# Optimization experiments

Measured on AMD Instinct MI355X. Metric: run time of the kernel, lower is better.

## Reference

```python
import jax, jax.numpy as jnp
import numpy as np

B, S, D, H = 4, 2048, 256, 8
HD = D // H  # 32
SCALE = 1.0 / jnp.sqrt(256.0)  # module divides by sqrt(256.0), NOT sqrt(head_dim)


def setup_inputs() -> dict:
    key = jax.random.key(0)
    ks = jax.random.split(key, 11)
    inp = {
        "q_in": jax.random.normal(ks[0], (B, S, D), jnp.float32),
        "k_in": jax.random.normal(ks[1], (B, S, D), jnp.float32),
        "v_in": jax.random.normal(ks[2], (B, S, D), jnp.float32),
        # causal mask, broadcastable over batch and heads; every row has >=1 one
        "mask": jnp.tril(jnp.ones((S, S), jnp.float32))[None, None, :, :],
        "Wq": jax.random.normal(ks[3], (D, D), jnp.float32) * 0.05,
        "bq": jnp.zeros((D,), jnp.float32),
        "Wk": jax.random.normal(ks[4], (D, D), jnp.float32) * 0.05,
        "bk": jnp.zeros((D,), jnp.float32),
        "Wv": jax.random.normal(ks[5], (D, D), jnp.float32) * 0.05,
        "bv": jnp.zeros((D,), jnp.float32),
        "Wo": jax.random.normal(ks[6], (D, D), jnp.float32) * 0.05,
        "bo": jnp.zeros((D,), jnp.float32),
    }
    return inp


def _mask_softmax(x, mask):
    # faithful to module: exp (no max-subtraction), remask, normalize
    e = jnp.exp(x) * mask
    return e / jnp.sum(e, axis=-1, keepdims=True)


def reference(q_in, k_in, v_in, mask, Wq, bq, Wk, bk, Wv, bv, Wo, bo):
    Q = (q_in @ Wq + bq).reshape(B, S, H, HD)
    K = (k_in @ Wk + bk).reshape(B, S, H, HD)
    V = (v_in @ Wv + bv).reshape(B, S, H, HD)
    scores = jnp.einsum("bqhd,bkhd->bhqk", Q, K) * SCALE  # [B,H,S,S]
    scores = scores * mask  # module multiplies mask into scores first
    p = _mask_softmax(scores, mask)
    attn = jnp.einsum("bhqk,bkhd->bqhd", p, V).reshape(B, S, D)
    return attn @ Wo + bo
```

## Files before the change

kernel.cpp:

```cpp
#include <hip/hip_runtime.h>
#include <hip/hip_bf16.h>

#define BATCH 4
#define S_LEN 2048
#define D_MOD 256
#define NH 8
#define HDIM 32
#define SCALE_ 0.0625f

typedef short bf16x8 __attribute__((ext_vector_type(8)));
typedef short short4v __attribute__((ext_vector_type(4)));
typedef float f32x4 __attribute__((ext_vector_type(4)));

__device__ __forceinline__ short f2bf(float f) {
    __hip_bfloat16 h = __float2bfloat16(f);
    return *reinterpret_cast<short*>(&h);
}

__global__ __launch_bounds__(256) void wtrans_kernel(
    const float* __restrict__ Wq, const float* __restrict__ Wk,
    const float* __restrict__ Wv, const float* __restrict__ Wo,
    short* __restrict__ WT)
{
    const int wsel = blockIdx.x;
    const int k0 = blockIdx.y * 8;
    const float* W = wsel == 0 ? Wq : (wsel == 1 ? Wk : (wsel == 2 ? Wv : Wo));
    short* T = WT + (size_t)wsel * 256 * 256;
    int n = threadIdx.x;
    bf16x8 o;
    #pragma unroll
    for (int kk = 0; kk < 8; ++kk)
        o[kk] = f2bf(W[(size_t)(k0 + kk) * 256 + n]);
    *(bf16x8*)&T[(size_t)n * 256 + k0] = o;
}

__global__ __launch_bounds__(256) void qkv_proj_kernel(
    const float* __restrict__ q_in, const float* __restrict__ k_in,
    const float* __restrict__ v_in, const short* __restrict__ WT,
    const float* __restrict__ bq, const float* __restrict__ bk,
    const float* __restrict__ bv,
    short* __restrict__ Qp, short* __restrict__ Kp, short* __restrict__ Vt)
{
    __shared__ short lsA[32][264];
    const int mt = blockIdx.x;
    const int seg = blockIdx.y;
    const float* A = seg == 0 ? q_in : (seg == 1 ? k_in : v_in);
    const short* WTs = WT + (size_t)seg * 65536;
    const float* bias = seg == 0 ? bq : (seg == 1 ? bk : bv);
    const int m0 = mt * 32;
    const int tid = threadIdx.x;

    {
        const float4* A4 = (const float4*)(A + (size_t)m0 * D_MOD);
        #pragma unroll
        for (int i = 0; i < 8; ++i) {
            int f4 = tid + i * 256;
            int row = f4 >> 6, c4 = f4 & 63;
            float4 v = A4[f4];
            short4v o;
            o.x = f2bf(v.x); o.y = f2bf(v.y); o.z = f2bf(v.z); o.w = f2bf(v.w);
            *(short4v*)&lsA[row][c4 * 4] = o;
        }
    }
    __syncthreads();

    const int w = tid >> 6, l = tid & 63, g = l >> 4, r15 = l & 15;
    bf16x8 af[2][8];
    #pragma unroll
    for (int f = 0; f < 2; ++f)
        #pragma unroll
        for (int kk = 0; kk < 8; ++kk)
            af[f][kk] = *(const bf16x8*)&lsA[f * 16 + r15][kk * 32 + 8 * g];

    const int bidx = m0 >> 11;
    const int s_base = m0 & (S_LEN - 1);

    #pragma unroll
    for (int ntl = 0; ntl < 4; ++ntl) {
        int col = w * 64 + ntl * 16 + r15;
        f32x4 acc0 = {}, acc1 = {};
        #pragma unroll
        for (int kk = 0; kk < 8; ++kk) {
            bf16x8 b = *(const bf16x8*)&WTs[(size_t)col * 256 + kk * 32 + 8 * g];
            acc0 = __builtin_amdgcn_mfma_f32_16x16x32_bf16(af[0][kk], b, acc0, 0, 0, 0);
            acc1 = __builtin_amdgcn_mfma_f32_16x16x32_bf16(af[1][kk], b, acc1, 0, 0, 0);
        }
        float bval = bias[col];
        int h = col >> 5, hd = col & 31;
        if (seg < 2) {
            short* Out = seg == 0 ? Qp : Kp;
            short* Outh = Out + ((size_t)(bidx * NH + h) * S_LEN) * HDIM;
            #pragma unroll
            for (int r = 0; r < 4; ++r) {
                int s0 = s_base + 4 * g + r;
                Outh[(size_t)s0 * HDIM + hd]        = f2bf(acc0[r] + bval);
                Outh[(size_t)(s0 + 16) * HDIM + hd] = f2bf(acc1[r] + bval);
            }
        } else {
            short* Vh = Vt + ((size_t)(bidx * NH + h) * HDIM + hd) * S_LEN;
            short4v o0, o1;
            #pragma unroll
            for (int r = 0; r < 4; ++r) { o0[r] = f2bf(acc0[r] + bval); o1[r] = f2bf(acc1[r] + bval); }
            size_t s = s_base + 4 * g;
            *(short4v*)&Vh[s]      = o0;
            *(short4v*)&Vh[s + 16] = o1;
        }
    }
}

__global__ __launch_bounds__(256) void attn_kernel(
    const short* __restrict__ Qp, const short* __restrict__ Kp,
    const short* __restrict__ Vt, short* __restrict__ Ab)
{
    __shared__ char smem[18432];
    __shared__ float psl[4][2][16];
    short (*pl)[32][72] = (short(*)[32][72])smem;
    float (*comb)[32][33] = (float(*)[32][33])smem;

    const int idx = blockIdx.x;
    const int bh = 4 * (idx & 7) + ((idx >> 3) & 3);
    const int jq = 63 - (idx >> 5);
    const int b = bh >> 3, h = bh & 7;
    const int tid = threadIdx.x;
    const int w = tid >> 6, l = tid & 63, g = l >> 4, r15 = l & 15;
    const int q0 = jq * 32;

    const short* Qph = Qp + (size_t)bh * S_LEN * HDIM;
    const short* Kph = Kp + (size_t)bh * S_LEN * HDIM;
    const short* Vtp = Vt + (size_t)bh * HDIM * S_LEN;

    bf16x8 aq0 = *(const bf16x8*)&Qph[(size_t)(q0 + r15) * HDIM + 8 * g];
    bf16x8 aq1 = *(const bf16x8*)&Qph[(size_t)(q0 + 16 + r15) * HDIM + 8 * g];

    f32x4 oacc[2][2] = {};
    float ps0[4] = {}, ps1[4] = {};
    const f32x4 zero = {};
    const int ntiles = (q0 + 95) >> 6;

    bf16x8 bkb[4];
    {
        const int k0 = w * 64;
        if (w < ntiles) {
            #pragma unroll
            for (int n = 0; n < 4; ++n)
                bkb[n] = *(const bf16x8*)&Kph[(size_t)(k0 + n * 16 + r15) * HDIM + 8 * g];
        }
    }

    for (int kt = w; kt < ntiles; kt += 4) {
        const int k0 = kt * 64;
        const bool full = (k0 + 63) <= q0;
        bf16x8 bkn[4];
        const int ktn = kt + 4;
        if (ktn < ntiles) {
            const int k0n = ktn * 64;
            #pragma unroll
            for (int n = 0; n < 4; ++n)
                bkn[n] = *(const bf16x8*)&Kph[(size_t)(k0n + n * 16 + r15) * HDIM + 8 * g];
        }

        __builtin_amdgcn_s_setprio(1);
        f32x4 s0v[4], s1v[4];
        #pragma unroll
        for (int n = 0; n < 4; ++n) {
            s0v[n] = __builtin_amdgcn_mfma_f32_16x16x32_bf16(aq0, bkb[n], zero, 0, 0, 0);
            s1v[n] = __builtin_amdgcn_mfma_f32_16x16x32_bf16(aq1, bkb[n], zero, 0, 0, 0);
        }
        __builtin_amdgcn_s_setprio(0);

        #pragma unroll
        for (int n = 0; n < 4; ++n) {
            int key = k0 + n * 16 + r15;
            if (full) {
                #pragma unroll
                for (int r = 0; r < 4; ++r) {
                    float e0 = __expf(s0v[n][r] * SCALE_);
                    float e1 = __expf(s1v[n][r] * SCALE_);
                    ps0[r] += e0; ps1[r] += e1;
                    pl[w][4 * g + r][n * 16 + r15]      = f2bf(e0);
                    pl[w][16 + 4 * g + r][n * 16 + r15] = f2bf(e1);
                }
            } else {
                #pragma unroll
                for (int r = 0; r < 4; ++r) {
                    int qr = q0 + 4 * g + r;
                    float e0 = (key <= qr)      ? __expf(s0v[n][r] * SCALE_) : 0.0f;
                    float e1 = (key <= qr + 16) ? __expf(s1v[n][r] * SCALE_) : 0.0f;
                    ps0[r] += e0; ps1[r] += e1;
                    pl[w][4 * g + r][n * 16 + r15]      = f2bf(e0);
                    pl[w][16 + 4 * g + r][n * 16 + r15] = f2bf(e1);
                }
            }
        }

        __builtin_amdgcn_s_setprio(1);
        #pragma unroll
        for (int ks = 0; ks < 2; ++ks) {
            bf16x8 pa0 = *(const bf16x8*)&pl[w][r15][ks * 32 + 8 * g];
            bf16x8 pa1 = *(const bf16x8*)&pl[w][16 + r15][ks * 32 + 8 * g];
            #pragma unroll
            for (int n2 = 0; n2 < 2; ++n2) {
                bf16x8 bv = *(const bf16x8*)&Vtp[(size_t)(n2 * 16 + r15) * S_LEN + k0 + ks * 32 + 8 * g];
                oacc[0][n2] = __builtin_amdgcn_mfma_f32_16x16x32_bf16(pa0, bv, oacc[0][n2], 0, 0, 0);
                oacc[1][n2] = __builtin_amdgcn_mfma_f32_16x16x32_bf16(pa1, bv, oacc[1][n2], 0, 0, 0);
            }
        }
        __builtin_amdgcn_s_setprio(0);

        if (ktn < ntiles) {
            #pragma unroll
            for (int n = 0; n < 4; ++n) bkb[n] = bkn[n];
        }
    }

    #pragma unroll
    for (int r = 0; r < 4; ++r) {
        float v0 = ps0[r], v1 = ps1[r];
        v0 += __shfl_xor(v0, 1); v1 += __shfl_xor(v1, 1);
        v0 += __shfl_xor(v0, 2); v1 += __shfl_xor(v1, 2);
        v0 += __shfl_xor(v0, 4); v1 += __shfl_xor(v1, 4);
        v0 += __shfl_xor(v0, 8); v1 += __shfl_xor(v1, 8);
        ps0[r] = v0; ps1[r] = v1;
    }

    __syncthreads();
    #pragma unroll
    for (int n2 = 0; n2 < 2; ++n2) {
        #pragma unroll
        for (int r = 0; r < 4; ++r) {
            comb[w][4 * g + r][n2 * 16 + r15]      = oacc[0][n2][r];
            comb[w][16 + 4 * g + r][n2 * 16 + r15] = oacc[1][n2][r];
        }
    }
    if (r15 == 0) {
        #pragma unroll
        for (int r = 0; r < 4; ++r) {
            psl[w][0][4 * g + r] = ps0[r];
            psl[w][1][4 * g + r] = ps1[r];
        }
    }
    __syncthreads();

    {
        int q = tid >> 3, hd0 = (tid & 7) * 4;
        int qf = q >> 4, q15 = q & 15;
        float ps = psl[0][qf][q15] + psl[1][qf][q15] + psl[2][qf][q15] + psl[3][qf][q15];
        float inv = __fdividef(1.0f, ps);
        short4v o;
        #pragma unroll
        for (int j = 0; j < 4; ++j) {
            float v = comb[0][q][hd0 + j] + comb[1][q][hd0 + j]
                    + comb[2][q][hd0 + j] + comb[3][q][hd0 + j];
            o[j] = f2bf(v * inv);
        }
        *(short4v*)&Ab[((size_t)b * S_LEN + q0 + q) * D_MOD + h * HDIM + hd0] = o;
    }
}

__global__ __launch_bounds__(256) void out_proj_kernel(
    const short* __restrict__ Ab, const short* __restrict__ WTo,
    const float* __restrict__ bo, float* __restrict__ out)
{
    const int m0 = blockIdx.x * 32;
    const int tid = threadIdx.x;
    const int w = tid >> 6, l = tid & 63, g = l >> 4, r15 = l & 15;

    bf16x8 af[2][8];
    #pragma unroll
    for (int f = 0; f < 2; ++f)
        #pragma unroll
        for (int kk = 0; kk < 8; ++kk)
            af[f][kk] = *(const bf16x8*)&Ab[(size_t)(m0 + f * 16 + r15) * D_MOD + kk * 32 + 8 * g];

    #pragma unroll
    for (int ntl = 0; ntl < 4; ++ntl) {
        int col = w * 64 + ntl * 16 + r15;
        f32x4 acc0 = {}, acc1 = {};
        #pragma unroll
        for (int kk = 0; kk < 8; ++kk) {
            bf16x8 bfr = *(const bf16x8*)&WTo[(size_t)col * 256 + kk * 32 + 8 * g];
            acc0 = __builtin_amdgcn_mfma_f32_16x16x32_bf16(af[0][kk], bfr, acc0, 0, 0, 0);
            acc1 = __builtin_amdgcn_mfma_f32_16x16x32_bf16(af[1][kk], bfr, acc1, 0, 0, 0);
        }
        float bval = bo[col];
        #pragma unroll
        for (int r = 0; r < 4; ++r) {
            out[(size_t)(m0 + 4 * g + r) * D_MOD + col]      = acc0[r] + bval;
            out[(size_t)(m0 + 16 + 4 * g + r) * D_MOD + col] = acc1[r] + bval;
        }
    }
}

extern "C" void kernel_launch(void* const* d_in, const int* in_sizes, int n_in,
                              void* d_out, int out_size, void* d_ws, size_t ws_size,
                              hipStream_t stream) {
    const float* q_in = (const float*)d_in[0];
    const float* k_in = (const float*)d_in[1];
    const float* v_in = (const float*)d_in[2];
    const float* Wq = (const float*)d_in[4];
    const float* bq = (const float*)d_in[5];
    const float* Wk = (const float*)d_in[6];
    const float* bk = (const float*)d_in[7];
    const float* Wv = (const float*)d_in[8];
    const float* bv = (const float*)d_in[9];
    const float* Wo = (const float*)d_in[10];
    const float* bo = (const float*)d_in[11];
    float* out = (float*)d_out;

    const size_t NTOK = (size_t)BATCH * S_LEN * D_MOD;
    short* WT = (short*)d_ws;
    short* Qp = WT + 4 * 65536;
    short* Kp = Qp + NTOK;
    short* Vt = Kp + NTOK;
    short* Ab = Vt + NTOK;

    wtrans_kernel<<<dim3(4, 32), 256, 0, stream>>>(Wq, Wk, Wv, Wo, WT);
    qkv_proj_kernel<<<dim3(256, 3), 256, 0, stream>>>(
        q_in, k_in, v_in, WT, bq, bk, bv, Qp, Kp, Vt);
    attn_kernel<<<2048, 256, 0, stream>>>(Qp, Kp, Vt, Ab);
    out_proj_kernel<<<256, 256, 0, stream>>>(Ab, WT + 3 * 65536, bo, out);
}
```

Baseline: 71.61 us.

## Pair long and short causal query tiles per block, fold scale into Q

Each attention block now handles two 32-row query tiles, one near the end and one near the start of the sequence, so causal work is balanced across blocks and each K/V tile load serves both tiles. The grid is halved to 1024 blocks. The softmax scale times log2(e) is folded into Q during projection so the inner loop can use exp2f without a multiply. The K double-buffer prefetch is removed and V loads are hoisted ahead of the PV MFMAs. This adds more LDS use and more registers per block, which could reduce occupancy, and Q is rounded to bf16 after scaling, which slightly changes precision.

```diff
diff --git a/kernel.cpp b/kernel.cpp
--- a/kernel.cpp
+++ b/kernel.cpp
@@ -7,6 +7,7 @@
 #define NH 8
 #define HDIM 32
 #define SCALE_ 0.0625f
+#define QLOG2E 0.09016844f
 
 typedef short bf16x8 __attribute__((ext_vector_type(8)));
 typedef short short4v __attribute__((ext_vector_type(4)));
@@ -87,9 +88,16 @@
         }
         float bval = bias[col];
         int h = col >> 5, hd = col & 31;
-        if (seg < 2) {
-            short* Out = seg == 0 ? Qp : Kp;
-            short* Outh = Out + ((size_t)(bidx * NH + h) * S_LEN) * HDIM;
+        if (seg == 0) {
+            short* Outh = Qp + ((size_t)(bidx * NH + h) * S_LEN) * HDIM;
+            #pragma unroll
+            for (int r = 0; r < 4; ++r) {
+                int s0 = s_base + 4 * g + r;
+                Outh[(size_t)s0 * HDIM + hd]        = f2bf((acc0[r] + bval) * QLOG2E);
+                Outh[(size_t)(s0 + 16) * HDIM + hd] = f2bf((acc1[r] + bval) * QLOG2E);
+            }
+        } else if (seg == 1) {
+            short* Outh = Kp + ((size_t)(bidx * NH + h) * S_LEN) * HDIM;
             #pragma unroll
             for (int r = 0; r < 4; ++r) {
                 int s0 = s_base + 4 * g + r;
@@ -108,152 +116,183 @@
     }
 }
 
-__global__ __launch_bounds__(256) void attn_kernel(
+__global__ __launch_bounds__(256, 4) void attn_kernel(
     const short* __restrict__ Qp, const short* __restrict__ Kp,
     const short* __restrict__ Vt, short* __restrict__ Ab)
 {
-    __shared__ char smem[18432];
-    __shared__ float psl[4][2][16];
-    short (*pl)[32][72] = (short(*)[32][72])smem;
-    float (*comb)[32][33] = (float(*)[32][33])smem;
+    __shared__ short pl[4][64][72];
+    __shared__ float psl[4][4][16];
+    float (*comb)[64][33] = (float(*)[64][33])pl;
 
     const int idx = blockIdx.x;
     const int bh = 4 * (idx & 7) + ((idx >> 3) & 3);
-    const int jq = 63 - (idx >> 5);
+    const int t  = idx >> 5;
     const int b = bh >> 3, h = bh & 7;
     const int tid = threadIdx.x;
     const int w = tid >> 6, l = tid & 63, g = l >> 4, r15 = l & 15;
-    const int q0 = jq * 32;
+    const int q0b = (63 - t) * 32;
+    const int q0s = t * 32;
 
     const short* Qph = Qp + (size_t)bh * S_LEN * HDIM;
     const short* Kph = Kp + (size_t)bh * S_LEN * HDIM;
     const short* Vtp = Vt + (size_t)bh * HDIM * S_LEN;
 
-    bf16x8 aq0 = *(const bf16x8*)&Qph[(size_t)(q0 + r15) * HDIM + 8 * g];
-    bf16x8 aq1 = *(const bf16x8*)&Qph[(size_t)(q0 + 16 + r15) * HDIM + 8 * g];
-
-    f32x4 oacc[2][2] = {};
-    float ps0[4] = {}, ps1[4] = {};
+    bf16x8 aqb0 = *(const bf16x8*)&Qph[(size_t)(q0b + r15) * HDIM + 8 * g];
+    bf16x8 aqb1 = *(const bf16x8*)&Qph[(size_t)(q0b + 16 + r15) * HDIM + 8 * g];
+    bf16x8 aqs0 = *(const bf16x8*)&Qph[(size_t)(q0s + r15) * HDIM + 8 * g];
+    bf16x8 aqs1 = *(const bf16x8*)&Qph[(size_t)(q0s + 16 + r15) * HDIM + 8 * g];
+
+    f32x4 ob[2][2] = {}, os[2][2] = {};
+    float psb0[4] = {}, psb1[4] = {}, pss0[4] = {}, pss1[4] = {};
     const f32x4 zero = {};
-    const int ntiles = (q0 + 95) >> 6;
-
-    bf16x8 bkb[4];
-    {
-        const int k0 = w * 64;
-        if (w < ntiles) {
-            #pragma unroll
-            for (int n = 0; n < 4; ++n)
-                bkb[n] = *(const bf16x8*)&Kph[(size_t)(k0 + n * 16 + r15) * HDIM + 8 * g];
-        }
-    }
-
-    for (int kt = w; kt < ntiles; kt += 4) {
+    const int ntb = (q0b + 95) >> 6;
+    const int nts = (q0s + 95) >> 6;
+
+    for (int kt = w; kt < ntb; kt += 4) {
         const int k0 = kt * 64;
-        const bool full = (k0 + 63) <= q0;
-        bf16x8 bkn[4];
-        const int ktn = kt + 4;
-        if (ktn < ntiles) {
-            const int k0n = ktn * 64;
-            #pragma unroll
-            for (int n = 0; n < 4; ++n)
-                bkn[n] = *(const bf16x8*)&Kph[(size_t)(k0n + n * 16 + r15) * HDIM + 8 * g];
-        }
-
-        __builtin_amdgcn_s_setprio(1);
-        f32x4 s0v[4], s1v[4];
+        const bool son = kt < nts;
+        const bool fb = (k0 + 63) <= q0b;
+        const bool fs = (k0 + 63) <= q0s;
+
+        bf16x8 bk[4];
+        #pragma unroll
+        for (int n = 0; n < 4; ++n)
+            bk[n] = *(const bf16x8*)&Kph[(size_t)(k0 + n * 16 + r15) * HDIM + 8 * g];
+
         #pragma unroll
         for (int n = 0; n < 4; ++n) {
-            s0v[n] = __builtin_amdgcn_mfma_f32_16x16x32_bf16(aq0, bkb[n], zero, 0, 0, 0);
-            s1v[n] = __builtin_amdgcn_mfma_f32_16x16x32_bf16(aq1, bkb[n], zero, 0, 0, 0);
-        }
-        __builtin_amdgcn_s_setprio(0);
-
-        #pragma unroll
-        for (int n = 0; n < 4; ++n) {
-            int key = k0 + n * 16 + r15;
-            if (full) {
+            const int key = k0 + n * 16 + r15;
+            __builtin_amdgcn_s_setprio(1);
+            f32x4 s0 = __builtin_amdgcn_mfma_f32_16x16x32_bf16(aqb0, bk[n], zero, 0, 0, 0);
+            f32x4 s1 = __builtin_amdgcn_mfma_f32_16x16x32_bf16(aqb1, bk[n], zero, 0, 0, 0);
+            __builtin_amdgcn_s_setprio(0);
+            if (fb) {
                 #pragma unroll
                 for (int r = 0; r < 4; ++r) {
-                    float e0 = __expf(s0v[n][r] * SCALE_);
-                    float e1 = __expf(s1v[n][r] * SCALE_);
-                    ps0[r] += e0; ps1[r] += e1;
+                    float e0 = exp2f(s0[r]);
+                    float e1 = exp2f(s1[r]);
+                    psb0[r] += e0; psb1[r] += e1;
                     pl[w][4 * g + r][n * 16 + r15]      = f2bf(e0);
                     pl[w][16 + 4 * g + r][n * 16 + r15] = f2bf(e1);
                 }
             } else {
                 #pragma unroll
                 for (int r = 0; r < 4; ++r) {
-                    int qr = q0 + 4 * g + r;
-                    float e0 = (key <= qr)      ? __expf(s0v[n][r] * SCALE_) : 0.0f;
-                    float e1 = (key <= qr + 16) ? __expf(s1v[n][r] * SCALE_) : 0.0f;
-                    ps0[r] += e0; ps1[r] += e1;
+                    int qr = q0b + 4 * g + r;
+                    float e0 = (key <= qr)      ? exp2f(s0[r]) : 0.0f;
+                    float e1 = (key <= qr + 16) ? exp2f(s1[r]) : 0.0f;
+                    psb0[r] += e0; psb1[r] += e1;
                     pl[w][4 * g + r][n * 16 + r15]      = f2bf(e0);
                     pl[w][16 + 4 * g + r][n * 16 + r15] = f2bf(e1);
                 }
             }
-        }
+            if (son) {
+                __builtin_amdgcn_s_setprio(1);
+                f32x4 u0 = __builtin_amdgcn_mfma_f32_16x16x32_bf16(aqs0, bk[n], zero, 0, 0, 0);
+                f32x4 u1 = __builtin_amdgcn_mfma_f32_16x16x32_bf16(aqs1, bk[n], zero, 0, 0, 0);
+                __builtin_amdgcn_s_setprio(0);
+                if (fs) {
+                    #pragma unroll
+                    for (int r = 0; r < 4; ++r) {
+                        float e0 = exp2f(u0[r]);
+                        float e1 = exp2f(u1[r]);
+                        pss0[r] += e0; pss1[r] += e1;
+                        pl[w][32 + 4 * g + r][n * 16 + r15] = f2bf(e0);
+                        pl[w][48 + 4 * g + r][n * 16 + r15] = f2bf(e1);
+                    }
+                } else {
+                    #pragma unroll
+                    for (int r = 0; r < 4; ++r) {
+                        int qr = q0s + 4 * g + r;
+                        float e0 = (key <= qr)      ? exp2f(u0[r]) : 0.0f;
+                        float e1 = (key <= qr + 16) ? exp2f(u1[r]) : 0.0f;
+                        pss0[r] += e0; pss1[r] += e1;
+                        pl[w][32 + 4 * g + r][n * 16 + r15] = f2bf(e0);
+                        pl[w][48 + 4 * g + r][n * 16 + r15] = f2bf(e1);
+                    }
+                }
+            }
+        }
+
+        bf16x8 bv[2][2];
+        #pragma unroll
+        for (int n2 = 0; n2 < 2; ++n2)
+            #pragma unroll
+            for (int ks = 0; ks < 2; ++ks)
+                bv[n2][ks] = *(const bf16x8*)&Vtp[(size_t)(n2 * 16 + r15) * S_LEN + k0 + ks * 32 + 8 * g];
 
         __builtin_amdgcn_s_setprio(1);
         #pragma unroll
         for (int ks = 0; ks < 2; ++ks) {
-            bf16x8 pa0 = *(const bf16x8*)&pl[w][r15][ks * 32 + 8 * g];
-            bf16x8 pa1 = *(const bf16x8*)&pl[w][16 + r15][ks * 32 + 8 * g];
+            bf16x8 pb0 = *(const bf16x8*)&pl[w][r15][ks * 32 + 8 * g];
+            bf16x8 pb1 = *(const bf16x8*)&pl[w][16 + r15][ks * 32 + 8 * g];
             #pragma unroll
             for (int n2 = 0; n2 < 2; ++n2) {
-                bf16x8 bv = *(const bf16x8*)&Vtp[(size_t)(n2 * 16 + r15) * S_LEN + k0 + ks * 32 + 8 * g];
-                oacc[0][n2] = __builtin_amdgcn_mfma_f32_16x16x32_bf16(pa0, bv, oacc[0][n2], 0, 0, 0);
-                oacc[1][n2] = __builtin_amdgcn_mfma_f32_16x16x32_bf16(pa1, bv, oacc[1][n2], 0, 0, 0);
+                ob[0][n2] = __builtin_amdgcn_mfma_f32_16x16x32_bf16(pb0, bv[n2][ks], ob[0][n2], 0, 0, 0);
+                ob[1][n2] = __builtin_amdgcn_mfma_f32_16x16x32_bf16(pb1, bv[n2][ks], ob[1][n2], 0, 0, 0);
+            }
+        }
+        if (son) {
+            #pragma unroll
+            for (int ks = 0; ks < 2; ++ks) {
+                bf16x8 pc0 = *(const bf16x8*)&pl[w][32 + r15][ks * 32 + 8 * g];
+                bf16x8 pc1 = *(const bf16x8*)&pl[w][48 + r15][ks * 32 + 8 * g];
+                #pragma unroll
+                for (int n2 = 0; n2 < 2; ++n2) {
+                    os[0][n2] = __builtin_amdgcn_mfma_f32_16x16x32_bf16(pc0, bv[n2][ks], os[0][n2], 0, 0, 0);
+                    os[1][n2] = __builtin_amdgcn_mfma_f32_16x16x32_bf16(pc1, bv[n2][ks], os[1][n2], 0, 0, 0);
+                }
             }
         }
         __builtin_amdgcn_s_setprio(0);
-
-        if (ktn < ntiles) {
-            #pragma unroll
-            for (int n = 0; n < 4; ++n) bkb[n] = bkn[n];
-        }
     }
 
     #pragma unroll
     for (int r = 0; r < 4; ++r) {
-        float v0 = ps0[r], v1 = ps1[r];
-        v0 += __shfl_xor(v0, 1); v1 += __shfl_xor(v1, 1);
-        v0 += __shfl_xor(v0, 2); v1 += __shfl_xor(v1, 2);
-        v0 += __shfl_xor(v0, 4); v1 += __shfl_xor(v1, 4);
-        v0 += __shfl_xor(v0, 8); v1 += __shfl_xor(v1, 8);
-        ps0[r] = v0; ps1[r] = v1;
-    }
-
+        float v0 = psb0[r], v1 = psb1[r], v2 = pss0[r], v3 = pss1[r];
+        v0 += __shfl_xor(v0, 1); v1 += __shfl_xor(v1, 1); v2 += __shfl_xor(v2, 1); v3 += __shfl_xor(v3, 1);
+        v0 += __shfl_xor(v0, 2); v1 += __shfl_xor(v1, 2); v2 += __shfl_xor(v2, 2); v3 += __shfl_xor(v3, 2);
+        v0 += __shfl_xor(v0, 4); v1 += __shfl_xor(v1, 4); v2 += __shfl_xor(v2, 4); v3 += __shfl_xor(v3, 4);
+        v0 += __shfl_xor(v0, 8); v1 += __shfl_xor(v1, 8); v2 += __shfl_xor(v2, 8); v3 += __shfl_xor(v3, 8);
+        psb0[r] = v0; psb1[r] = v1; pss0[r] = v2; pss1[r] = v3;
+    }
+    if (r15 == 0) {
+        #pragma unroll
+        for (int r = 0; r < 4; ++r) {
+            psl[w][0][4 * g + r] = psb0[r];
+            psl[w][1][4 * g + r] = psb1[r];
+            psl[w][2][4 * g + r] = pss0[r];
+            psl[w][3][4 * g + r] = pss1[r];
+        }
+    }
     __syncthreads();
+
     #pragma unroll
     for (int n2 = 0; n2 < 2; ++n2) {
         #pragma unroll
         for (int r = 0; r < 4; ++r) {
-            comb[w][4 * g + r][n2 * 16 + r15]      = oacc[0][n2][r];
-            comb[w][16 + 4 * g + r][n2 * 16 + r15] = oacc[1][n2][r];
-        }
-    }
-    if (r15 == 0) {
-        #pragma unroll
-        for (int r = 0; r < 4; ++r) {
-            psl[w][0][4 * g + r] = ps0[r];
-            psl[w][1][4 * g + r] = ps1[r];
+            comb[w][4 * g + r][n2 * 16 + r15]      = ob[0][n2][r];
+            comb[w][16 + 4 * g + r][n2 * 16 + r15] = ob[1][n2][r];
+            comb[w][32 + 4 * g + r][n2 * 16 + r15] = os[0][n2][r];
+            comb[w][48 + 4 * g + r][n2 * 16 + r15] = os[1][n2][r];
         }
     }
     __syncthreads();
 
     {
-        int q = tid >> 3, hd0 = (tid & 7) * 4;
-        int qf = q >> 4, q15 = q & 15;
-        float ps = psl[0][qf][q15] + psl[1][qf][q15] + psl[2][qf][q15] + psl[3][qf][q15];
+        int q = tid >> 2, hd0 = (tid & 3) * 8;
+        float ps = psl[0][q >> 4][q & 15] + psl[1][q >> 4][q & 15]
+                 + psl[2][q >> 4][q & 15] + psl[3][q >> 4][q & 15];
         float inv = __fdividef(1.0f, ps);
-        short4v o;
-        #pragma unroll
-        for (int j = 0; j < 4; ++j) {
+        int row = (q < 32) ? (q0b + q) : (q0s + q - 32);
+        bf16x8 o;
+        #pragma unroll
+        for (int j = 0; j < 8; ++j) {
             float v = comb[0][q][hd0 + j] + comb[1][q][hd0 + j]
                     + comb[2][q][hd0 + j] + comb[3][q][hd0 + j];
             o[j] = f2bf(v * inv);
         }
-        *(short4v*)&Ab[((size_t)b * S_LEN + q0 + q) * D_MOD + h * HDIM + hd0] = o;
+        *(bf16x8*)&Ab[((size_t)b * S_LEN + row) * D_MOD + h * HDIM + hd0] = o;
     }
 }
 
@@ -317,6 +356,6 @@
     wtrans_kernel<<<dim3(4, 32), 256, 0, stream>>>(Wq, Wk, Wv, Wo, WT);
     qkv_proj_kernel<<<dim3(256, 3), 256, 0, stream>>>(
         q_in, k_in, v_in, WT, bq, bk, bv, Qp, Kp, Vt);
-    attn_kernel<<<2048, 256, 0, stream>>>(Qp, Kp, Vt, Ab);
+    attn_kernel<<<1024, 256, 0, stream>>>(Qp, Kp, Vt, Ab);
     out_proj_kernel<<<256, 256, 0, stream>>>(Ab, WT + 3 * 65536, bo, out);
 }
```

Result: slower. 87.67 us (+22.4%).
